# Optimization experiments

Hardware: AMD Instinct MI355X
Metric: run time of the kernel (lower is better)

Reference implementation:

```python
import jax, jax.numpy as jnp
import numpy as np

PAD = 1
NMS_DIST = 4
BORDER_DIST = 4
TOP_K = 500
DET_THRESH = 0.8


def _conv(x, w, b, pad):
    y = jax.lax.conv_general_dilated(
        x, w, window_strides=(1, 1), padding=[(pad, pad), (pad, pad)],
        dimension_numbers=("NCHW", "OIHW", "NCHW"))
    return y + b[None, :, None, None]


def setup_inputs() -> dict:
    key = jax.random.key(0)
    ks = jax.random.split(key, 10)
    B, C, H, W = 2, 1, 384, 384

    def w(k, o, i, s):
        return jax.random.normal(k, (o, i, s, s), jnp.float32) * (1.0 / np.sqrt(i * s * s))

    return {
        "images": jax.random.uniform(ks[0], (B, C, H, W), jnp.float32),
        "bb_w1": w(ks[1], 64, 1, 3), "bb_b1": jnp.zeros((64,), jnp.float32),
        "bb_w2": w(ks[2], 64, 64, 3), "bb_b2": jnp.zeros((64,), jnp.float32),
        "bb_w3": w(ks[3], 128, 64, 3), "bb_b3": jnp.zeros((128,), jnp.float32),
        "bb_w4": w(ks[4], 128, 128, 3), "bb_b4": jnp.zeros((128,), jnp.float32),
        "det_w1": w(ks[5], 128, 128, 3), "det_b1": jnp.zeros((128,), jnp.float32),
        "det_w2": w(ks[6], 1, 128, 1), "det_b2": jnp.zeros((1,), jnp.float32),
        "des_w1": w(ks[7], 256, 128, 3), "des_b1": jnp.zeros((256,), jnp.float32),
        "des_w2": w(ks[8], 128, 256, 1), "des_b2": jnp.zeros((128,), jnp.float32),
        "scale_factor": jnp.float32(1.0),
    }


def reference(images, bb_w1, bb_b1, bb_w2, bb_b2, bb_w3, bb_b3, bb_w4, bb_b4,
              det_w1, det_b1, det_w2, det_b2, des_w1, des_b1, des_w2, des_b2,
              scale_factor):
    relu = jax.nn.relu
    x = relu(_conv(images, bb_w1, bb_b1, PAD))
    x = relu(_conv(x, bb_w2, bb_b2, PAD))
    x = relu(_conv(x, bb_w3, bb_b3, PAD))
    feats = relu(_conv(x, bb_w4, bb_b4, PAD))  # [B,128,H,W]

    # Detector head: 3x3 conv+ReLU, then 1x1 conv -> logits [B,1,H,W]
    d = relu(_conv(feats, det_w1, det_b1, PAD))
    logits = _conv(d, det_w2, det_b2, 0)

    # Descriptor head: 3x3 conv+ReLU (lat=256), then 1x1 conv -> raw descriptors [B,D,H,W]
    e = relu(_conv(feats, des_w1, des_b1, PAD))
    raw = _conv(e, des_w2, des_b2, 0)

    # MagicPoint post-processing (cell_size=1): prob = sigmoid(logits)
    prob = jax.nn.sigmoid(logits[:, 0])  # [B,H,W]
    B, H, W = prob.shape

    # Box NMS via max-pool: keep local maxima above threshold, suppress borders
    win = 2 * NMS_DIST + 1
    pooled = jax.lax.reduce_window(prob, -jnp.inf, jax.lax.max,
                                   (1, win, win), (1, 1, 1), "SAME")
    ys = jnp.arange(H)
    xs = jnp.arange(W)
    border = ((ys >= BORDER_DIST) & (ys < H - BORDER_DIST))[:, None] \
           & ((xs >= BORDER_DIST) & (xs < W - BORDER_DIST))[None, :]
    nms_prob = jnp.where((prob >= pooled) & (prob > DET_THRESH) & border, prob, 0.0)

    # Fixed top-k keypoints per image
    flat = nms_prob.reshape(B, H * W)
    topv, topi = jax.lax.top_k(flat, TOP_K)  # [B,K]
    y = (topi // W).astype(jnp.float32)
    xp = (topi % W).astype(jnp.float32)
    positions = jnp.stack([y, xp, topv], axis=-1)  # [B,K,3] (row, col, prob)

    # sparsify_descriptors: gather raw descriptors at keypoint locations, L2-normalize
    D = raw.shape[1]
    raw_flat = raw.reshape(B, D, H * W)
    desc = jnp.take_along_axis(raw_flat, topi[:, None, :], axis=2)  # [B,D,K]
    desc = jnp.swapaxes(desc, 1, 2)  # [B,K,D]
    norm = jnp.maximum(jnp.linalg.norm(desc, axis=-1, keepdims=True), 1e-12)
    sparse_descriptors = scale_factor * desc / norm
    return sparse_descriptors, positions
```

## Files before the change

### kernel.cpp

```cpp
#include <hip/hip_runtime.h>
#include <hip/hip_bf16.h>

#define DEVI __device__ __forceinline__

typedef __bf16 bf16x8 __attribute__((ext_vector_type(8)));
typedef float  f32x4  __attribute__((ext_vector_type(4)));
typedef unsigned short ushort_t;

static constexpr int H = 384, W = 384, BATCH = 2, HW = H * W;
static constexpr int NMSD = 4, BORD = 4, TOPK = 500;
static constexpr float THRESH = 0.8f;
static constexpr int CAP = 2048;
static constexpr int SORTN = 2048;

DEVI ushort_t f2b(float f) {
  __hip_bfloat16 h = __float2bfloat16(f);
  ushort_t s;
  __builtin_memcpy(&s, &h, 2);
  return s;
}
DEVI float b2f(ushort_t u) { return __uint_as_float(((unsigned)u) << 16); }

DEVI void gload_lds16(const void* g, void* l) {
  __builtin_amdgcn_global_load_lds((const __attribute__((address_space(1))) void*)g,
                                   (__attribute__((address_space(3))) void*)l,
                                   16, 0, 0);
}

DEVI void repack9(const float* __restrict__ src, ushort_t* __restrict__ dst,
                  int d, int O, int I) {
  int t = d / (O * I);
  int r = d % (O * I);
  int o = r / I, i = r % I;
  dst[d] = f2b(src[(o * I + i) * 9 + t]);
}

__global__ __launch_bounds__(256) void setup_all(
    const float* __restrict__ w2s, ushort_t* __restrict__ wp2,
    const float* __restrict__ w3s, ushort_t* __restrict__ wp3,
    const float* __restrict__ w4s, ushort_t* __restrict__ wp4,
    const float* __restrict__ wds, ushort_t* __restrict__ wpd,
    const float* __restrict__ dw1, ushort_t* __restrict__ w1t,
    const float* __restrict__ dw2, float* __restrict__ w2t,
    ushort_t* __restrict__ zer, int* __restrict__ cnt) {
  int d = blockIdx.x * 256 + threadIdx.x;
  if (d < 1024) { zer[d] = 0; if (d < 2) cnt[d] = 0; return; }
  d -= 1024;
  if (d < 36864)  { repack9(w2s, wp2, d, 64, 64);   return; }
  d -= 36864;
  if (d < 73728)  { repack9(w3s, wp3, d, 128, 64);  return; }
  d -= 73728;
  if (d < 147456) { repack9(w4s, wp4, d, 128, 128); return; }
  d -= 147456;
  if (d < 147456) { repack9(wds, wpd, d, 128, 128); return; }
  d -= 147456;
  if (d < 294912) {
    int o = d / 1152, k = d % 1152;
    w1t[(size_t)(k >> 2) * 1024 + o * 4 + (k & 3)] = f2b(dw1[d]);
    return;
  }
  d -= 294912;
  if (d < 32768) {
    int o = d / 128, c = d % 128;
    w2t[d] = dw2[c * 256 + o];
  }
}

__global__ __launch_bounds__(256) void conv1_kernel(
    const float* __restrict__ img, const float* __restrict__ w,
    const float* __restrict__ bias, ushort_t* __restrict__ xout) {
  __shared__ __align__(16) float wt[9 * 64];
  __shared__ float bs[64];
  const int tid = threadIdx.x;
  for (int j = tid; j < 576; j += 256) {
    int co = j / 9, t = j % 9;
    wt[t * 64 + co] = w[j];
  }
  if (tid < 64) bs[tid] = bias[tid];
  __syncthreads();

  const int p = blockIdx.x * 256 + tid;
  const int b = p / HW, rem = p % HW;
  const int y = rem / W, x = rem % W;

  float in[9];
#pragma unroll
  for (int t = 0; t < 9; ++t) {
    int yy = y + t / 3 - 1, xx = x + t % 3 - 1;
    in[t] = (yy >= 0 && yy < H && xx >= 0 && xx < W) ? img[(size_t)b * HW + yy * W + xx] : 0.f;
  }
  float acc[64];
#pragma unroll
  for (int c = 0; c < 64; ++c) acc[c] = bs[c];
#pragma unroll
  for (int t = 0; t < 9; ++t) {
    float v = in[t];
#pragma unroll
    for (int c4 = 0; c4 < 16; ++c4) {
      float4 w4 = *reinterpret_cast<const float4*>(&wt[t * 64 + c4 * 4]);
      acc[c4 * 4 + 0] += w4.x * v;
      acc[c4 * 4 + 1] += w4.y * v;
      acc[c4 * 4 + 2] += w4.z * v;
      acc[c4 * 4 + 3] += w4.w * v;
    }
  }
  ushort_t* op = xout + (size_t)p * 64;
#pragma unroll
  for (int g = 0; g < 8; ++g) {
    uint4 u;
    u.x = (unsigned)f2b(fmaxf(acc[g * 8 + 0], 0.f)) | ((unsigned)f2b(fmaxf(acc[g * 8 + 1], 0.f)) << 16);
    u.y = (unsigned)f2b(fmaxf(acc[g * 8 + 2], 0.f)) | ((unsigned)f2b(fmaxf(acc[g * 8 + 3], 0.f)) << 16);
    u.z = (unsigned)f2b(fmaxf(acc[g * 8 + 4], 0.f)) | ((unsigned)f2b(fmaxf(acc[g * 8 + 5], 0.f)) << 16);
    u.w = (unsigned)f2b(fmaxf(acc[g * 8 + 6], 0.f)) | ((unsigned)f2b(fmaxf(acc[g * 8 + 7], 0.f)) << 16);
    *reinterpret_cast<uint4*>(op + g * 8) = u;
  }
}

template <int CIN, int COUT, int MFRAG, int NFRAG>
__global__ __launch_bounds__(256) void conv3x3_mfma(
    const ushort_t* __restrict__ xin, const ushort_t* __restrict__ wp,
    const float* __restrict__ bias, ushort_t* __restrict__ xout,
    const ushort_t* __restrict__ zer) {
  constexpr int NT = 128;
  constexpr int BROWS = 144;
  constexpr int CC = CIN / 32;
  constexpr int P = 3 * CC;
  constexpr int ACH3 = 3 * COUT / 16;
  constexpr int APW = ACH3 / 4;

  __shared__ __align__(16) ushort_t lA[2][3 * COUT * 32];
  __shared__ __align__(16) ushort_t lB[2][BROWS * 32];

  const int x0 = (blockIdx.x % (W / NT)) * NT;
  const int y = blockIdx.x / (W / NT);
  const int b = blockIdx.y;

  const int tid = threadIdx.x;
  const int wid = tid >> 6, lane = tid & 63;
  const int wr = wid >> 1, wc = wid & 1;
  const int l4 = lane >> 2;
  const int lb8 = (lane & 3) * 8;
  const int kg = lane >> 4;
  const int lr = lane & 15;

  const f32x4 fz = {0.f, 0.f, 0.f, 0.f};
  f32x4 acc[MFRAG][NFRAG];
#pragma unroll
  for (int m = 0; m < MFRAG; ++m)
#pragma unroll
    for (int n = 0; n < NFRAG; ++n) acc[m][n] = fz;

  auto stage = [&](int p) {
    const int dyi = p / CC, ccc = p % CC, pb = p & 1;
    const int yy = y + dyi - 1;
    const bool rowok = (yy >= 0) && (yy < H);
    const ushort_t* srow = xin + ((size_t)(b * H + yy) * W) * CIN + ccc * 32;
#pragma unroll
    for (int j = 0; j < APW; ++j) {
      int ch = wid * APW + j;
      int row = ch * 16 + l4;
      int tt = row / COUT, co = row % COUT;
      const ushort_t* src =
          wp + ((size_t)(dyi * 3 + tt) * COUT + co) * CIN + ccc * 32 + lb8;
      gload_lds16(src, &lA[pb][ch * 512]);
    }
    for (int ch = wid; ch < 9; ch += 4) {
      int row = ch * 16 + l4;
      int xx = x0 - 1 + row;
      const ushort_t* src = (rowok && row < 130 && xx >= 0 && xx < W)
                                ? srow + (size_t)xx * CIN + lb8
                                : zer + lb8;
      gload_lds16(src, &lB[pb][ch * 512]);
    }
  };

  stage(0);
#pragma unroll 1
  for (int p = 0; p < P; ++p) {
    __syncthreads();
    if (p + 1 < P) stage(p + 1);
    const int pb = p & 1;
#pragma unroll
    for (int tt = 0; tt < 3; ++tt) {
      bf16x8 af[MFRAG], bfr[NFRAG];
#pragma unroll
      for (int m = 0; m < MFRAG; ++m)
        af[m] = *reinterpret_cast<const bf16x8*>(
            &lA[pb][(tt * COUT + wr * MFRAG * 16 + m * 16 + lr) * 32 + kg * 8]);
#pragma unroll
      for (int n = 0; n < NFRAG; ++n)
        bfr[n] = *reinterpret_cast<const bf16x8*>(
            &lB[pb][(wc * NFRAG * 16 + n * 16 + lr + tt) * 32 + kg * 8]);
#pragma unroll
      for (int m = 0; m < MFRAG; ++m)
#pragma unroll
        for (int n = 0; n < NFRAG; ++n)
          acc[m][n] = __builtin_amdgcn_mfma_f32_16x16x32_bf16(af[m], bfr[n], acc[m][n], 0, 0, 0);
    }
  }

  const int lq = lane >> 4;
  ushort_t* orow = xout + ((size_t)(b * H + y) * W) * COUT;
#pragma unroll
  for (int m = 0; m < MFRAG; ++m) {
    const int co = wr * MFRAG * 16 + m * 16 + lq * 4;
    const float4 bv = *reinterpret_cast<const float4*>(&bias[co]);
#pragma unroll
    for (int n = 0; n < NFRAG; ++n) {
      const int px = x0 + wc * NFRAG * 16 + n * 16 + lr;
      f32x4 v = acc[m][n];
      ushort4 pk;
      pk.x = f2b(fmaxf(v[0] + bv.x, 0.f));
      pk.y = f2b(fmaxf(v[1] + bv.y, 0.f));
      pk.z = f2b(fmaxf(v[2] + bv.z, 0.f));
      pk.w = f2b(fmaxf(v[3] + bv.w, 0.f));
      *reinterpret_cast<ushort4*>(&orow[(size_t)px * COUT + co]) = pk;
    }
  }
}

__global__ __launch_bounds__(384) void det2_rowmax(
    const ushort_t* __restrict__ dbuf, const float* __restrict__ w2,
    const float* __restrict__ b2, float* __restrict__ prob,
    float* __restrict__ tmp) {
  __shared__ float ws[128];
  __shared__ float pr[W];
  const int tid = threadIdx.x;
  if (tid < 128) ws[tid] = w2[tid];
  __syncthreads();
  const int p = blockIdx.x * W + tid;
  const ushort_t* dp = dbuf + (size_t)p * 128;
  float acc = b2[0];
#pragma unroll
  for (int k = 0; k < 128; k += 8) {
    uint4 q = *reinterpret_cast<const uint4*>(dp + k);
    acc += __uint_as_float(q.x << 16) * ws[k + 0];
    acc += __uint_as_float(q.x & 0xffff0000u) * ws[k + 1];
    acc += __uint_as_float(q.y << 16) * ws[k + 2];
    acc += __uint_as_float(q.y & 0xffff0000u) * ws[k + 3];
    acc += __uint_as_float(q.z << 16) * ws[k + 4];
    acc += __uint_as_float(q.z & 0xffff0000u) * ws[k + 5];
    acc += __uint_as_float(q.w << 16) * ws[k + 6];
    acc += __uint_as_float(q.w & 0xffff0000u) * ws[k + 7];
  }
  float pv = 1.f / (1.f + expf(-acc));
  prob[p] = pv;
  pr[tid] = pv;
  __syncthreads();
  float m = -1e30f;
#pragma unroll
  for (int d = -NMSD; d <= NMSD; ++d) {
    int xx = tid + d;
    if (xx >= 0 && xx < W) m = fmaxf(m, pr[xx]);
  }
  tmp[p] = m;
}

__global__ __launch_bounds__(256) void colmax9_cand(
    const float* __restrict__ tmp, const float* __restrict__ prob,
    int* __restrict__ cnt, float* __restrict__ candv, int* __restrict__ candi) {
  const int p = blockIdx.x * 256 + threadIdx.x;
  const int b = p / HW, rem = p % HW;
  const int y = rem / W, x = rem % W;
  float m = -1e30f;
#pragma unroll
  for (int d = -NMSD; d <= NMSD; ++d) {
    int yy = y + d;
    if (yy >= 0 && yy < H) m = fmaxf(m, tmp[(size_t)b * HW + yy * W + x]);
  }
  float pv = prob[p];
  bool keep = (pv >= m) && (pv > THRESH) &&
              (y >= BORD) && (y < H - BORD) && (x >= BORD) && (x < W - BORD);
  if (keep) {
    int pos = atomicAdd(&cnt[b], 1);
    if (pos < CAP) {
      candv[b * CAP + pos] = pv;
      candi[b * CAP + pos] = rem;
    }
  }
}

__global__ __launch_bounds__(256) void select_topk(
    const int* __restrict__ cnt, const float* __restrict__ candv,
    const int* __restrict__ candi, float* __restrict__ pos_out,
    int* __restrict__ topi_g) {
  __shared__ float sv[SORTN];
  __shared__ int si[SORTN];
  __shared__ int tail[TOPK];
  const int b = blockIdx.x, tid = threadIdx.x;
  int nc = cnt[b];
  if (nc > CAP) nc = CAP;
  for (int j = tid; j < SORTN; j += 256) {
    if (j < nc) {
      sv[j] = candv[b * CAP + j];
      si[j] = candi[b * CAP + j];
    } else {
      sv[j] = -1.f;
      si[j] = 0x7fffffff;
    }
  }
  __syncthreads();
  if (nc > 0) {
    for (int k = 2; k <= SORTN; k <<= 1) {
      for (int j = k >> 1; j > 0; j >>= 1) {
        for (int i = tid; i < SORTN; i += 256) {
          int l = i ^ j;
          if (l > i) {
            float vi = sv[i], vl = sv[l];
            int ii = si[i], il = si[l];
            bool i_better = (vi > vl) || (vi == vl && ii < il);
            bool desc = ((i & k) == 0);
            bool sw = desc ? (!i_better) : i_better;
            if (sw) {
              sv[i] = vl; sv[l] = vi;
              si[i] = il; si[l] = ii;
            }
          }
        }
        __syncthreads();
      }
    }
  }
  if (tid == 0) {
    int need = TOPK - nc;
    if (need < 0) need = 0;
    int idx = 0, filled = 0;
    while (filled < need && idx < HW) {
      bool used = false;
      for (int q = 0; q < nc; ++q)
        if (si[q] == idx) { used = true; break; }
      if (!used) tail[filled++] = idx;
      ++idx;
    }
  }
  __syncthreads();
  for (int k2 = tid; k2 < TOPK; k2 += 256) {
    float v; int idx;
    if (k2 < nc) { v = sv[k2]; idx = si[k2]; }
    else         { v = 0.f;    idx = tail[k2 - nc]; }
    pos_out[((size_t)b * TOPK + k2) * 3 + 0] = (float)(idx / W);
    pos_out[((size_t)b * TOPK + k2) * 3 + 1] = (float)(idx % W);
    pos_out[((size_t)b * TOPK + k2) * 3 + 2] = v;
    topi_g[b * TOPK + k2] = idx;
  }
}

__global__ __launch_bounds__(256) void des_head(
    const ushort_t* __restrict__ feats, const int* __restrict__ topi_g,
    const ushort_t* __restrict__ w1t, const float* __restrict__ b1,
    const float* __restrict__ w2t, const float* __restrict__ b2,
    const float* __restrict__ scale, float* __restrict__ desc_out) {
  __shared__ __align__(16) float xf[1152];
  __shared__ __align__(16) float es[256];
  __shared__ float rs[128];
  __shared__ float nrm_s;
  const int g = blockIdx.x;
  const int b = g / TOPK;
  const int tid = threadIdx.x;
  const int idx = topi_g[g];
  const int y = idx / W, x = idx % W;
  for (int j = tid; j < 1152; j += 256) {
    int ci = j / 9, t = j % 9;
    int yy = y + t / 3 - 1, xx = x + t % 3 - 1;
    xf[j] = (yy >= 0 && yy < H && xx >= 0 && xx < W)
                ? b2f(feats[((size_t)(b * H + yy) * W + xx) * 128 + ci])
                : 0.f;
  }
  __syncthreads();
  float e = b1[tid];
  const ushort4* w4p = reinterpret_cast<const ushort4*>(w1t);
#pragma unroll 4
  for (int k4 = 0; k4 < 288; ++k4) {
    ushort4 wv = w4p[(size_t)k4 * 256 + tid];
    float4 x4 = *reinterpret_cast<const float4*>(&xf[k4 * 4]);
    e += b2f(wv.x) * x4.x + b2f(wv.y) * x4.y + b2f(wv.z) * x4.z + b2f(wv.w) * x4.w;
  }
  es[tid] = fmaxf(e, 0.f);
  __syncthreads();
  if (tid < 128) {
    float r = b2[tid];
#pragma unroll 4
    for (int o = 0; o < 256; ++o) r += es[o] * w2t[o * 128 + tid];
    rs[tid] = r;
  }
  __syncthreads();
  if (tid < 64) {
    float v = rs[tid] * rs[tid] + rs[tid + 64] * rs[tid + 64];
    for (int off = 32; off > 0; off >>= 1) v += __shfl_down(v, off);
    if (tid == 0) nrm_s = sqrtf(v);
  }
  __syncthreads();
  if (tid < 128) {
    float nrm = fmaxf(nrm_s, 1e-12f);
    desc_out[(size_t)g * 128 + tid] = rs[tid] * (scale[0] / nrm);
  }
}

extern "C" void kernel_launch(void* const* d_in, const int* in_sizes, int n_in,
                              void* d_out, int out_size, void* d_ws, size_t ws_size,
                              hipStream_t stream) {
  (void)in_sizes; (void)n_in; (void)out_size; (void)ws_size;
  const float* images = (const float*)d_in[0];
  const float* bbw1 = (const float*)d_in[1];  const float* bbb1 = (const float*)d_in[2];
  const float* bbw2 = (const float*)d_in[3];  const float* bbb2 = (const float*)d_in[4];
  const float* bbw3 = (const float*)d_in[5];  const float* bbb3 = (const float*)d_in[6];
  const float* bbw4 = (const float*)d_in[7];  const float* bbb4 = (const float*)d_in[8];
  const float* dtw1 = (const float*)d_in[9];  const float* dtb1 = (const float*)d_in[10];
  const float* dtw2 = (const float*)d_in[11]; const float* dtb2 = (const float*)d_in[12];
  const float* dsw1 = (const float*)d_in[13]; const float* dsb1 = (const float*)d_in[14];
  const float* dsw2 = (const float*)d_in[15]; const float* dsb2 = (const float*)d_in[16];
  const float* scale = (const float*)d_in[17];

  char* ws = (char*)d_ws;
  constexpr size_t SZ64 = (size_t)BATCH * HW * 64 * 2;
  constexpr size_t SZ128 = (size_t)BATCH * HW * 128 * 2;

  ushort_t* x1   = (ushort_t*)ws;
  ushort_t* x2   = (ushort_t*)(ws + SZ64);
  ushort_t* x3   = (ushort_t*)(ws + SZ128);
  ushort_t* fts  = (ushort_t*)ws;
  ushort_t* dbuf = (ushort_t*)(ws + SZ128);

  size_t off = 2 * SZ128;
  auto alloc = [&](size_t bytes) {
    char* p = ws + off;
    off = (off + bytes + 255) & ~(size_t)255;
    return p;
  };
  float* prob = (float*)alloc((size_t)BATCH * HW * 4);
  float* tmp  = (float*)alloc((size_t)BATCH * HW * 4);
  ushort_t* wp2 = (ushort_t*)alloc(9 * 64 * 64 * 2);
  ushort_t* wp3 = (ushort_t*)alloc(9 * 128 * 64 * 2);
  ushort_t* wp4 = (ushort_t*)alloc(9 * 128 * 128 * 2);
  ushort_t* wpd = (ushort_t*)alloc(9 * 128 * 128 * 2);
  ushort_t* w1t = (ushort_t*)alloc(288 * 256 * 4 * 2);
  float*    w2t = (float*)alloc(256 * 128 * 4);
  ushort_t* zer = (ushort_t*)alloc(2048);
  int* cnt      = (int*)alloc(256);
  float* candv  = (float*)alloc((size_t)BATCH * CAP * 4);
  int* candi    = (int*)alloc((size_t)BATCH * CAP * 4);
  int* topi_g   = (int*)alloc((size_t)BATCH * TOPK * 4);

  float* desc_out = (float*)d_out;
  float* pos_out  = (float*)d_out + (size_t)BATCH * TOPK * 128;

  setup_all<<<2868, 256, 0, stream>>>(bbw2, wp2, bbw3, wp3, bbw4, wp4, dtw1, wpd,
                                      dsw1, w1t, dsw2, w2t, zer, cnt);

  conv1_kernel<<<BATCH * HW / 256, 256, 0, stream>>>(images, bbw1, bbb1, x1);
  conv3x3_mfma<64, 64, 2, 4>  <<<dim3(3 * H, BATCH), 256, 0, stream>>>(x1, wp2, bbb2, x2, zer);
  conv3x3_mfma<64, 128, 4, 4> <<<dim3(3 * H, BATCH), 256, 0, stream>>>(x2, wp3, bbb3, x3, zer);
  conv3x3_mfma<128, 128, 4, 4><<<dim3(3 * H, BATCH), 256, 0, stream>>>(x3, wp4, bbb4, fts, zer);
  conv3x3_mfma<128, 128, 4, 4><<<dim3(3 * H, BATCH), 256, 0, stream>>>(fts, wpd, dtb1, dbuf, zer);

  det2_rowmax<<<BATCH * H, 384, 0, stream>>>(dbuf, dtw2, dtb2, prob, tmp);
  colmax9_cand<<<BATCH * HW / 256, 256, 0, stream>>>(tmp, prob, cnt, candv, candi);
  select_topk<<<BATCH, 256, 0, stream>>>(cnt, candv, candi, pos_out, topi_g);
  des_head<<<BATCH * TOPK, 256, 0, stream>>>(fts, topi_g, w1t, dsb1, w2t, dsb2, scale, desc_out);
}
```

Before: 547.5 us.

## Widen conv tiles to 192 pixels, drop double buffering, reorder descriptor weights

The MFMA 3x3 conv kernel now takes the pixel-tile width as a template parameter. The three 128-output-channel layers use 192-pixel tiles with six N fragments, which reuses each weight tile across more pixels. Double-buffered LDS staging is replaced by a single buffer with two barriers per K step, and launch bounds now ask for 3 blocks per CU. This frees LDS and registers for occupancy but gives up load/compute overlap inside a block. The descriptor head's weight layout and feature gather are reordered tap-major, so consecutive threads read consecutive channels for coalesced access.

Result: slower. 745.2 us (+36.1%).

```diff
diff --git a/kernel.cpp b/kernel.cpp
--- a/kernel.cpp
+++ b/kernel.cpp
@@ -56,7 +56,8 @@
   d -= 147456;
   if (d < 294912) {
     int o = d / 1152, k = d % 1152;
-    w1t[(size_t)(k >> 2) * 1024 + o * 4 + (k & 3)] = f2b(dw1[d]);
+    int kp = (k % 9) * 128 + (k / 9);
+    w1t[(size_t)(kp >> 2) * 1024 + o * 4 + (kp & 3)] = f2b(dw1[d]);
     return;
   }
   d -= 294912;
@@ -116,20 +117,18 @@
   }
 }
 
-template <int CIN, int COUT, int MFRAG, int NFRAG>
-__global__ __launch_bounds__(256) void conv3x3_mfma(
+template <int CIN, int COUT, int MFRAG, int NFRAG, int NT>
+__global__ __launch_bounds__(256, 3) void conv3x3_mfma(
     const ushort_t* __restrict__ xin, const ushort_t* __restrict__ wp,
     const float* __restrict__ bias, ushort_t* __restrict__ xout,
     const ushort_t* __restrict__ zer) {
-  constexpr int NT = 128;
-  constexpr int BROWS = 144;
   constexpr int CC = CIN / 32;
-  constexpr int P = 3 * CC;
   constexpr int ACH3 = 3 * COUT / 16;
   constexpr int APW = ACH3 / 4;
-
-  __shared__ __align__(16) ushort_t lA[2][3 * COUT * 32];
-  __shared__ __align__(16) ushort_t lB[2][BROWS * 32];
+  constexpr int BCH = (NT + 2 + 15) / 16;
+
+  __shared__ __align__(16) ushort_t lA[3 * COUT * 32];
+  __shared__ __align__(16) ushort_t lB[BCH * 16 * 32];
 
   const int x0 = (blockIdx.x % (W / NT)) * NT;
   const int y = blockIdx.x / (W / NT);
@@ -150,52 +149,49 @@
 #pragma unroll
     for (int n = 0; n < NFRAG; ++n) acc[m][n] = fz;
 
-  auto stage = [&](int p) {
-    const int dyi = p / CC, ccc = p % CC, pb = p & 1;
-    const int yy = y + dyi - 1;
+#pragma unroll 1
+  for (int dy = -1; dy <= 1; ++dy) {
+    const int yy = y + dy;
     const bool rowok = (yy >= 0) && (yy < H);
-    const ushort_t* srow = xin + ((size_t)(b * H + yy) * W) * CIN + ccc * 32;
-#pragma unroll
-    for (int j = 0; j < APW; ++j) {
-      int ch = wid * APW + j;
-      int row = ch * 16 + l4;
-      int tt = row / COUT, co = row % COUT;
-      const ushort_t* src =
-          wp + ((size_t)(dyi * 3 + tt) * COUT + co) * CIN + ccc * 32 + lb8;
-      gload_lds16(src, &lA[pb][ch * 512]);
-    }
-    for (int ch = wid; ch < 9; ch += 4) {
-      int row = ch * 16 + l4;
-      int xx = x0 - 1 + row;
-      const ushort_t* src = (rowok && row < 130 && xx >= 0 && xx < W)
-                                ? srow + (size_t)xx * CIN + lb8
-                                : zer + lb8;
-      gload_lds16(src, &lB[pb][ch * 512]);
-    }
-  };
-
-  stage(0);
+    const ushort_t* srow = xin + ((size_t)(b * H + yy) * W) * CIN;
 #pragma unroll 1
-  for (int p = 0; p < P; ++p) {
-    __syncthreads();
-    if (p + 1 < P) stage(p + 1);
-    const int pb = p & 1;
-#pragma unroll
-    for (int tt = 0; tt < 3; ++tt) {
-      bf16x8 af[MFRAG], bfr[NFRAG];
-#pragma unroll
-      for (int m = 0; m < MFRAG; ++m)
-        af[m] = *reinterpret_cast<const bf16x8*>(
-            &lA[pb][(tt * COUT + wr * MFRAG * 16 + m * 16 + lr) * 32 + kg * 8]);
-#pragma unroll
-      for (int n = 0; n < NFRAG; ++n)
-        bfr[n] = *reinterpret_cast<const bf16x8*>(
-            &lB[pb][(wc * NFRAG * 16 + n * 16 + lr + tt) * 32 + kg * 8]);
-#pragma unroll
-      for (int m = 0; m < MFRAG; ++m)
+    for (int cc = 0; cc < CIN; cc += 32) {
+#pragma unroll
+      for (int j = 0; j < APW; ++j) {
+        int ch = wid * APW + j;
+        int row = ch * 16 + l4;
+        int tt = row / COUT, co = row % COUT;
+        const ushort_t* src =
+            wp + ((size_t)((dy + 1) * 3 + tt) * COUT + co) * CIN + cc + lb8;
+        gload_lds16(src, &lA[ch * 512]);
+      }
+      for (int ch = wid; ch < BCH; ch += 4) {
+        int row = ch * 16 + l4;
+        int xx = x0 - 1 + row;
+        const ushort_t* src = (rowok && row < NT + 2 && xx >= 0 && xx < W)
+                                  ? srow + (size_t)xx * CIN + cc + lb8
+                                  : zer + lb8;
+        gload_lds16(src, &lB[ch * 512]);
+      }
+      __syncthreads();
+#pragma unroll
+      for (int tt = 0; tt < 3; ++tt) {
+        bf16x8 af[MFRAG], bfr[NFRAG];
+#pragma unroll
+        for (int m = 0; m < MFRAG; ++m)
+          af[m] = *reinterpret_cast<const bf16x8*>(
+              &lA[(tt * COUT + wr * MFRAG * 16 + m * 16 + lr) * 32 + kg * 8]);
 #pragma unroll
         for (int n = 0; n < NFRAG; ++n)
-          acc[m][n] = __builtin_amdgcn_mfma_f32_16x16x32_bf16(af[m], bfr[n], acc[m][n], 0, 0, 0);
+          bfr[n] = *reinterpret_cast<const bf16x8*>(
+              &lB[(wc * NFRAG * 16 + n * 16 + lr + tt) * 32 + kg * 8]);
+#pragma unroll
+        for (int m = 0; m < MFRAG; ++m)
+#pragma unroll
+          for (int n = 0; n < NFRAG; ++n)
+            acc[m][n] = __builtin_amdgcn_mfma_f32_16x16x32_bf16(af[m], bfr[n], acc[m][n], 0, 0, 0);
+      }
+      __syncthreads();
     }
   }
 
@@ -360,7 +356,7 @@
   const int idx = topi_g[g];
   const int y = idx / W, x = idx % W;
   for (int j = tid; j < 1152; j += 256) {
-    int ci = j / 9, t = j % 9;
+    int t = j >> 7, ci = j & 127;
     int yy = y + t / 3 - 1, xx = x + t % 3 - 1;
     xf[j] = (yy >= 0 && yy < H && xx >= 0 && xx < W)
                 ? b2f(feats[((size_t)(b * H + yy) * W + xx) * 128 + ci])
@@ -448,10 +444,10 @@
                                       dsw1, w1t, dsw2, w2t, zer, cnt);
 
   conv1_kernel<<<BATCH * HW / 256, 256, 0, stream>>>(images, bbw1, bbb1, x1);
-  conv3x3_mfma<64, 64, 2, 4>  <<<dim3(3 * H, BATCH), 256, 0, stream>>>(x1, wp2, bbb2, x2, zer);
-  conv3x3_mfma<64, 128, 4, 4> <<<dim3(3 * H, BATCH), 256, 0, stream>>>(x2, wp3, bbb3, x3, zer);
-  conv3x3_mfma<128, 128, 4, 4><<<dim3(3 * H, BATCH), 256, 0, stream>>>(x3, wp4, bbb4, fts, zer);
-  conv3x3_mfma<128, 128, 4, 4><<<dim3(3 * H, BATCH), 256, 0, stream>>>(fts, wpd, dtb1, dbuf, zer);
+  conv3x3_mfma<64, 64, 2, 4, 128>  <<<dim3(3 * H, BATCH), 256, 0, stream>>>(x1, wp2, bbb2, x2, zer);
+  conv3x3_mfma<64, 128, 4, 6, 192> <<<dim3(2 * H, BATCH), 256, 0, stream>>>(x2, wp3, bbb3, x3, zer);
+  conv3x3_mfma<128, 128, 4, 6, 192><<<dim3(2 * H, BATCH), 256, 0, stream>>>(x3, wp4, bbb4, fts, zer);
+  conv3x3_mfma<128, 128, 4, 6, 192><<<dim3(2 * H, BATCH), 256, 0, stream>>>(fts, wpd, dtb1, dbuf, zer);
 
   det2_rowmax<<<BATCH * H, 384, 0, stream>>>(dbuf, dtw2, dtb2, prob, tmp);
   colmax9_cand<<<BATCH * HW / 256, 256, 0, stream>>>(tmp, prob, cnt, candv, candi);
```
